# Kernel tuning notes

Hardware: AMD Instinct MI355X
Metric: run time of the kernel (lower is better)

The kernel has to match this reference:

```python
import jax, jax.numpy as jnp
import numpy as np

B, S, D = 64, 64, 2048          # NOTE: repo's RoPE transpose requires B == S
H, KVH, HD = 8, 1, 256
INTER = 16384
EPS = 1e-6
ROPE_THETA = 10000.0


def setup_inputs() -> dict:
    key = jax.random.key(0)
    ks = jax.random.split(key, 10)
    sc = 0.02
    hidden_states = jax.random.normal(ks[0], (B, S, D), jnp.float32)
    causal = jnp.tril(jnp.ones((S, S), dtype=bool))
    attention_mask = jnp.broadcast_to(
        jnp.where(causal, 0.0, -1e9).astype(jnp.float32)[None, None], (B, 1, S, S))
    position_ids = jnp.broadcast_to(jnp.arange(S, dtype=jnp.int32)[None, :], (B, S))
    inv_freq = 1.0 / (ROPE_THETA ** (jnp.arange(0, HD, 2, dtype=jnp.float32) / HD))
    return {
        "hidden_states": hidden_states,
        "attention_mask": attention_mask,
        "position_ids": position_ids,
        "inv_freq": inv_freq,
        "wq": sc * jax.random.normal(ks[1], (H * HD, D), jnp.float32),
        "wk": sc * jax.random.normal(ks[2], (KVH * HD, D), jnp.float32),
        "wv": sc * jax.random.normal(ks[3], (KVH * HD, D), jnp.float32),
        "wo": sc * jax.random.normal(ks[4], (D, H * HD), jnp.float32),
        "w_gate": sc * jax.random.normal(ks[5], (INTER, D), jnp.float32),
        "w_up": sc * jax.random.normal(ks[6], (INTER, D), jnp.float32),
        "w_down": sc * jax.random.normal(ks[7], (D, INTER), jnp.float32),
        "ln1_w": sc * jax.random.normal(ks[8], (D,), jnp.float32),
        "ln2_w": sc * jax.random.normal(ks[9], (D,), jnp.float32),
    }


def _rms_norm(x, w):
    xf = x.astype(jnp.float32)
    out = xf * jax.lax.rsqrt(jnp.mean(xf * xf, axis=-1, keepdims=True) + EPS)
    return (out * (1.0 + w.astype(jnp.float32))).astype(x.dtype)


def _rotate_half(x):
    x1, x2 = jnp.split(x, 2, axis=-1)
    return jnp.concatenate((-x2, x1), axis=-1)


def _decoder_layer(hidden_states, attention_mask, position_ids, inv_freq,
                   wq, wk, wv, wo, w_gate, w_up, w_down, ln1_w, ln2_w):
    residual = hidden_states
    h = _rms_norm(hidden_states, ln1_w)

    # projections -> (B, heads, S, HD)
    q = (h @ wq.T).reshape(B, S, H, HD).transpose(0, 2, 1, 3)
    k = (h @ wk.T).reshape(B, S, KVH, HD).transpose(0, 2, 1, 3)
    v = (h @ wv.T).reshape(B, S, KVH, HD).transpose(0, 2, 1, 3)

    # rotary embeddings: freqs (B, S, HD/2) -> emb (B, S, HD)
    freqs = jnp.einsum('d,bs->bsd', inv_freq, position_ids.astype(jnp.float32))
    emb = jnp.concatenate((freqs, freqs), axis=-1)
    cos, sin = jnp.cos(emb), jnp.sin(emb)
    # faithful to repo: unsqueeze(1) then transpose dims 0<->2 -> (S, 1, B, HD)
    ct = jnp.transpose(cos[:, None], (2, 1, 0, 3))
    st = jnp.transpose(sin[:, None], (2, 1, 0, 3))
    q = q * ct + _rotate_half(q) * st
    k = k * ct + _rotate_half(k) * st

    # repeat_kv: MQA -> full heads
    k = jnp.repeat(k, H // KVH, axis=1)
    v = jnp.repeat(v, H // KVH, axis=1)

    scores = jnp.einsum('bhqd,bhkd->bhqk', q, k) / np.sqrt(HD).astype(np.float32)
    scores = scores + attention_mask
    # softmax computed in float16, then cast back (matches torch code)
    attn = jax.nn.softmax(scores.astype(jnp.float16), axis=-1).astype(q.dtype)

    out = jnp.einsum('bhqk,bhkd->bhqd', attn, v)
    out = out.transpose(0, 2, 1, 3).reshape(B, S, H * HD) @ wo.T
    hidden_states = residual + out

    residual = hidden_states
    h2 = _rms_norm(hidden_states, ln2_w)
    mlp = (jax.nn.gelu(h2 @ w_gate.T, approximate=True) * (h2 @ w_up.T)) @ w_down.T
    hidden_states = residual + mlp
    return hidden_states, attn


def reference(hidden_states, attention_mask, position_ids, inv_freq,
              wq, wk, wv, wo, w_gate, w_up, w_down, ln1_w, ln2_w):
    return _decoder_layer(hidden_states, attention_mask, position_ids, inv_freq,
                          wq, wk, wv, wo, w_gate, w_up, w_down, ln1_w, ln2_w)
```

## Files before the change

kernel.cpp:

```cpp
#include <hip/hip_runtime.h>
#include <hip/hip_fp16.h>

typedef _Float16 half8 __attribute__((ext_vector_type(8)));
typedef _Float16 half4v __attribute__((ext_vector_type(4)));
typedef float floatx4 __attribute__((ext_vector_type(4)));

constexpr int BATCH = 64, SEQ = 64, DM = 2048, NHEAD = 8, HDIM = 256, FF = 16384;

__device__ __forceinline__ float f16r(float x) { return (float)(_Float16)x; }

__global__ __launch_bounds__(256) void rmsnorm_kernel(
    const float* __restrict__ x, const float* __restrict__ w, _Float16* __restrict__ out) {
  const int row = blockIdx.x;
  const float4* xr = (const float4*)(x + (size_t)row * DM);
  const int tid = threadIdx.x;
  float4 a = xr[tid];
  float4 b = xr[tid + 256];
  float s = a.x*a.x + a.y*a.y + a.z*a.z + a.w*a.w
          + b.x*b.x + b.y*b.y + b.z*b.z + b.w*b.w;
  #pragma unroll
  for (int off = 32; off > 0; off >>= 1) s += __shfl_xor(s, off, 64);
  __shared__ float ps[4];
  if ((tid & 63) == 0) ps[tid >> 6] = s;
  __syncthreads();
  const float rs = rsqrtf((ps[0] + ps[1] + ps[2] + ps[3]) * (1.0f / DM) + 1e-6f);
  const float4* wr = (const float4*)w;
  float4 w1 = wr[tid], w2 = wr[tid + 256];
  half4v o1, o2;
  o1[0] = (_Float16)(a.x * rs * (1.f + w1.x));
  o1[1] = (_Float16)(a.y * rs * (1.f + w1.y));
  o1[2] = (_Float16)(a.z * rs * (1.f + w1.z));
  o1[3] = (_Float16)(a.w * rs * (1.f + w1.w));
  o2[0] = (_Float16)(b.x * rs * (1.f + w2.x));
  o2[1] = (_Float16)(b.y * rs * (1.f + w2.y));
  o2[2] = (_Float16)(b.z * rs * (1.f + w2.z));
  o2[3] = (_Float16)(b.w * rs * (1.f + w2.w));
  half4v* op = (half4v*)(out + (size_t)row * DM);
  op[tid] = o1;
  op[tid + 256] = o2;
}

template<int EPI>
__global__ __launch_bounds__(256, 2) void gemm_f16(
    const _Float16* __restrict__ A, const float* __restrict__ Bw,
    float* C, const float* Res, int N, int K) {
  const int m0 = blockIdx.x * 128;
  const int n0 = blockIdx.y * 128;
  __shared__ _Float16 As[128 * 40];
  __shared__ _Float16 Bs[128 * 40];
  const int tid = threadIdx.x;
  const int lane = tid & 63;
  const int wave = tid >> 6;
  const int wm = (wave >> 1) * 64, wn = (wave & 1) * 64;
  const int lr = lane & 15, lk = (lane >> 4) * 8;
  const int r2 = tid >> 1, kh = (tid & 1) * 16;
  const _Float16* Ag = A + (size_t)(m0 + r2) * K + kh;
  const float* Bg = Bw + (size_t)(n0 + r2) * K + kh;
  _Float16* AsW = &As[r2 * 40 + kh];
  _Float16* BsW = &Bs[r2 * 40 + kh];
  floatx4 acc[4][4];
  #pragma unroll
  for (int i = 0; i < 4; ++i)
    #pragma unroll
    for (int j = 0; j < 4; ++j) acc[i][j] = (floatx4){0.f, 0.f, 0.f, 0.f};

  for (int kt = 0; kt < K; kt += 32) {
    float4 a0 = *(const float4*)(Ag);
    float4 a1 = *(const float4*)(Ag + 8);
    float4 b0 = *(const float4*)(Bg);
    float4 b1 = *(const float4*)(Bg + 4);
    float4 b2 = *(const float4*)(Bg + 8);
    float4 b3 = *(const float4*)(Bg + 12);
    Ag += 32; Bg += 32;
    half8 hb0, hb1;
    hb0[0]=(_Float16)b0.x; hb0[1]=(_Float16)b0.y; hb0[2]=(_Float16)b0.z; hb0[3]=(_Float16)b0.w;
    hb0[4]=(_Float16)b1.x; hb0[5]=(_Float16)b1.y; hb0[6]=(_Float16)b1.z; hb0[7]=(_Float16)b1.w;
    hb1[0]=(_Float16)b2.x; hb1[1]=(_Float16)b2.y; hb1[2]=(_Float16)b2.z; hb1[3]=(_Float16)b2.w;
    hb1[4]=(_Float16)b3.x; hb1[5]=(_Float16)b3.y; hb1[6]=(_Float16)b3.z; hb1[7]=(_Float16)b3.w;
    __syncthreads();
    *(float4*)AsW = a0;
    *(float4*)(AsW + 8) = a1;
    *(half8*)BsW = hb0;
    *(half8*)(BsW + 8) = hb1;
    __syncthreads();
    half8 af[4], bfr[4];
    #pragma unroll
    for (int i = 0; i < 4; ++i) af[i] = *(const half8*)&As[(wm + i * 16 + lr) * 40 + lk];
    #pragma unroll
    for (int j = 0; j < 4; ++j) bfr[j] = *(const half8*)&Bs[(wn + j * 16 + lr) * 40 + lk];
    #pragma unroll
    for (int i = 0; i < 4; ++i)
      #pragma unroll
      for (int j = 0; j < 4; ++j)
        acc[i][j] = __builtin_amdgcn_mfma_f32_16x16x32_f16(af[i], bfr[j], acc[i][j], 0, 0, 0);
  }
  const int mb = m0 + wm + (lane >> 4) * 4;
  const int nb = n0 + wn + (lane & 15);
  #pragma unroll
  for (int i = 0; i < 4; ++i)
    #pragma unroll
    for (int j = 0; j < 4; ++j)
      #pragma unroll
      for (int r = 0; r < 4; ++r) {
        size_t idx = (size_t)(mb + i * 16 + r) * N + (nb + j * 16);
        float val = acc[i][j][r];
        if constexpr (EPI == 1) val += Res[idx];
        C[idx] = val;
      }
}

__device__ __forceinline__ float gelu_tanh(float x) {
  float x3 = x * x * x;
  float t = tanhf(0.7978845608028654f * (x + 0.044715f * x3));
  return 0.5f * x * (1.0f + t);
}

__global__ __launch_bounds__(256, 2) void gemm_gateup(
    const _Float16* __restrict__ A, const float* __restrict__ Wg,
    const float* __restrict__ Wu, _Float16* __restrict__ Act) {
  const int K = DM, N = FF;
  const int m0 = blockIdx.x * 128;
  const int n0 = blockIdx.y * 128;
  __shared__ _Float16 As[128 * 40];
  __shared__ _Float16 Bgs[128 * 40];
  __shared__ _Float16 Bus[128 * 40];
  const int tid = threadIdx.x;
  const int lane = tid & 63;
  const int wave = tid >> 6;
  const int wm = (wave >> 1) * 64, wn = (wave & 1) * 64;
  const int lr = lane & 15, lk = (lane >> 4) * 8;
  const int r2 = tid >> 1, kh = (tid & 1) * 16;
  const _Float16* Ag = A + (size_t)(m0 + r2) * K + kh;
  const float* Bgg = Wg + (size_t)(n0 + r2) * K + kh;
  const float* Bgu = Wu + (size_t)(n0 + r2) * K + kh;
  _Float16* AsW = &As[r2 * 40 + kh];
  _Float16* BgW = &Bgs[r2 * 40 + kh];
  _Float16* BuW = &Bus[r2 * 40 + kh];
  floatx4 ag[4][4], au[4][4];
  #pragma unroll
  for (int i = 0; i < 4; ++i)
    #pragma unroll
    for (int j = 0; j < 4; ++j) {
      ag[i][j] = (floatx4){0.f, 0.f, 0.f, 0.f};
      au[i][j] = (floatx4){0.f, 0.f, 0.f, 0.f};
    }
  for (int kt = 0; kt < K; kt += 32) {
    float4 a0 = *(const float4*)(Ag);
    float4 a1 = *(const float4*)(Ag + 8);
    float4 g0 = *(const float4*)(Bgg);
    float4 g1 = *(const float4*)(Bgg + 4);
    float4 g2 = *(const float4*)(Bgg + 8);
    float4 g3 = *(const float4*)(Bgg + 12);
    float4 u0 = *(const float4*)(Bgu);
    float4 u1 = *(const float4*)(Bgu + 4);
    float4 u2 = *(const float4*)(Bgu + 8);
    float4 u3 = *(const float4*)(Bgu + 12);
    Ag += 32; Bgg += 32; Bgu += 32;
    half8 hg0, hg1, hu0, hu1;
    hg0[0]=(_Float16)g0.x; hg0[1]=(_Float16)g0.y; hg0[2]=(_Float16)g0.z; hg0[3]=(_Float16)g0.w;
    hg0[4]=(_Float16)g1.x; hg0[5]=(_Float16)g1.y; hg0[6]=(_Float16)g1.z; hg0[7]=(_Float16)g1.w;
    hg1[0]=(_Float16)g2.x; hg1[1]=(_Float16)g2.y; hg1[2]=(_Float16)g2.z; hg1[3]=(_Float16)g2.w;
    hg1[4]=(_Float16)g3.x; hg1[5]=(_Float16)g3.y; hg1[6]=(_Float16)g3.z; hg1[7]=(_Float16)g3.w;
    hu0[0]=(_Float16)u0.x; hu0[1]=(_Float16)u0.y; hu0[2]=(_Float16)u0.z; hu0[3]=(_Float16)u0.w;
    hu0[4]=(_Float16)u1.x; hu0[5]=(_Float16)u1.y; hu0[6]=(_Float16)u1.z; hu0[7]=(_Float16)u1.w;
    hu1[0]=(_Float16)u2.x; hu1[1]=(_Float16)u2.y; hu1[2]=(_Float16)u2.z; hu1[3]=(_Float16)u2.w;
    hu1[4]=(_Float16)u3.x; hu1[5]=(_Float16)u3.y; hu1[6]=(_Float16)u3.z; hu1[7]=(_Float16)u3.w;
    __syncthreads();
    *(float4*)AsW = a0;
    *(float4*)(AsW + 8) = a1;
    *(half8*)BgW = hg0; *(half8*)(BgW + 8) = hg1;
    *(half8*)BuW = hu0; *(half8*)(BuW + 8) = hu1;
    __syncthreads();
    half8 af[4], bg[4], bu[4];
    #pragma unroll
    for (int i = 0; i < 4; ++i) af[i] = *(const half8*)&As[(wm + i * 16 + lr) * 40 + lk];
    #pragma unroll
    for (int j = 0; j < 4; ++j) {
      bg[j] = *(const half8*)&Bgs[(wn + j * 16 + lr) * 40 + lk];
      bu[j] = *(const half8*)&Bus[(wn + j * 16 + lr) * 40 + lk];
    }
    #pragma unroll
    for (int i = 0; i < 4; ++i)
      #pragma unroll
      for (int j = 0; j < 4; ++j) {
        ag[i][j] = __builtin_amdgcn_mfma_f32_16x16x32_f16(af[i], bg[j], ag[i][j], 0, 0, 0);
        au[i][j] = __builtin_amdgcn_mfma_f32_16x16x32_f16(af[i], bu[j], au[i][j], 0, 0, 0);
      }
  }
  const int mb = m0 + wm + (lane >> 4) * 4;
  const int nb = n0 + wn + (lane & 15);
  #pragma unroll
  for (int i = 0; i < 4; ++i)
    #pragma unroll
    for (int j = 0; j < 4; ++j)
      #pragma unroll
      for (int r = 0; r < 4; ++r) {
        size_t idx = (size_t)(mb + i * 16 + r) * FF + (nb + j * 16);
        Act[idx] = (_Float16)(gelu_tanh(ag[i][j][r]) * au[i][j][r]);
      }
}

__global__ __launch_bounds__(256) void rope_kernel(
    float* __restrict__ x, const int* __restrict__ pos_ids,
    const float* __restrict__ inv_freq, int nh, int total) {
  int tid = blockIdx.x * 256 + threadIdx.x;
  if (tid >= total) return;
  int i = tid & 127;
  int rest = tid >> 7;
  int hh = rest % nh;
  int m = rest / nh;
  int b = m >> 6, s = m & 63;
  int pos = pos_ids[s * 64 + b];
  float fr = inv_freq[i] * (float)pos;
  float c = cosf(fr), sn = sinf(fr);
  size_t base = (size_t)m * ((size_t)nh * 256) + (size_t)hh * 256 + i;
  float x1 = x[base], x2 = x[base + 128];
  x[base] = x1 * c - x2 * sn;
  x[base + 128] = x2 * c + x1 * sn;
}

__global__ __launch_bounds__(256) void attn_kernel(
    const float* __restrict__ q, const float* __restrict__ k, const float* __restrict__ v,
    const float* __restrict__ mask, float* __restrict__ attn_out, _Float16* __restrict__ ctx) {
  const int bh = blockIdx.x;
  const int b = bh >> 3, h = bh & 7;
  __shared__ __align__(16) char smem[65536];
  const int tid = threadIdx.x;
  for (int it = 0; it < 16; ++it) {
    int f = it * 256 + tid;
    int t = f >> 6, d4 = f & 63;
    float4 kv = *(const float4*)(k + (size_t)(b * 64 + t) * HDIM + d4 * 4);
    int col = d4 ^ ((t >> 2) & 7);
    *(float4*)(smem + t * 1024 + col * 16) = kv;
  }
  __syncthreads();
  const int sg = tid >> 4, tg = tid & 15;
  const int s0 = sg * 4, t0 = tg * 4;
  float sc[4][4] = {};
  const float* qb = q + (size_t)(b * 64 + s0) * DM + h * HDIM;
  for (int d4 = 0; d4 < 64; ++d4) {
    float4 kvv[4];
    int col = d4 ^ (tg & 7);
    #pragma unroll
    for (int j = 0; j < 4; ++j)
      kvv[j] = *(const float4*)(smem + (t0 + j) * 1024 + col * 16);
    #pragma unroll
    for (int i = 0; i < 4; ++i) {
      float4 qv = *(const float4*)(qb + (size_t)i * DM + d4 * 4);
      #pragma unroll
      for (int j = 0; j < 4; ++j)
        sc[i][j] += qv.x * kvv[j].x + qv.y * kvv[j].y + qv.z * kvv[j].z + qv.w * kvv[j].w;
    }
  }
  float a16[4][4];
  const float* mrow = mask + (size_t)b * SEQ * SEQ;
  #pragma unroll
  for (int i = 0; i < 4; ++i) {
    const float4 mk = *(const float4*)(mrow + (size_t)(s0 + i) * SEQ + t0);
    float xh[4];
    xh[0] = f16r(sc[i][0] * 0.0625f + mk.x);
    xh[1] = f16r(sc[i][1] * 0.0625f + mk.y);
    xh[2] = f16r(sc[i][2] * 0.0625f + mk.z);
    xh[3] = f16r(sc[i][3] * 0.0625f + mk.w);
    float mx = fmaxf(fmaxf(xh[0], xh[1]), fmaxf(xh[2], xh[3]));
    #pragma unroll
    for (int off = 1; off < 16; off <<= 1) mx = fmaxf(mx, __shfl_xor(mx, off, 64));
    float ssum = 0.f;
    #pragma unroll
    for (int j = 0; j < 4; ++j) {
      float e = f16r(expf(f16r(xh[j] - mx)));
      a16[i][j] = e;
      ssum += e;
    }
    #pragma unroll
    for (int off = 1; off < 16; off <<= 1) ssum += __shfl_xor(ssum, off, 64);
    #pragma unroll
    for (int j = 0; j < 4; ++j) a16[i][j] = f16r(a16[i][j] / ssum);
  }
  float* ab = attn_out + (size_t)bh * SEQ * SEQ;
  #pragma unroll
  for (int i = 0; i < 4; ++i) {
    float4 av = {a16[i][0], a16[i][1], a16[i][2], a16[i][3]};
    *(float4*)(ab + (size_t)(s0 + i) * SEQ + t0) = av;
  }
  __syncthreads();
  float* as = (float*)smem;
  _Float16* vs = (_Float16*)(smem + 64 * 65 * 4);
  #pragma unroll
  for (int i = 0; i < 4; ++i)
    #pragma unroll
    for (int j = 0; j < 4; ++j)
      as[(s0 + i) * 65 + t0 + j] = a16[i][j];
  for (int it = 0; it < 16; ++it) {
    int f = it * 256 + tid;
    int t = f >> 6, d4 = f & 63;
    float4 vv = *(const float4*)(v + (size_t)(b * 64 + t) * HDIM + d4 * 4);
    half4v hv;
    hv[0] = (_Float16)vv.x; hv[1] = (_Float16)vv.y;
    hv[2] = (_Float16)vv.z; hv[3] = (_Float16)vv.w;
    *(half4v*)(vs + t * 264 + d4 * 4) = hv;
  }
  __syncthreads();
  floatx4 outv[4][4];
  #pragma unroll
  for (int i = 0; i < 4; ++i)
    #pragma unroll
    for (int u = 0; u < 4; ++u) outv[i][u] = (floatx4){0.f, 0.f, 0.f, 0.f};
  for (int t = 0; t < 64; ++t) {
    float av[4];
    #pragma unroll
    for (int i = 0; i < 4; ++i) av[i] = as[(s0 + i) * 65 + t];
    #pragma unroll
    for (int u = 0; u < 4; ++u) {
      half4v vh = *(const half4v*)(vs + t * 264 + tg * 4 + u * 64);
      floatx4 vf = {(float)vh[0], (float)vh[1], (float)vh[2], (float)vh[3]};
      #pragma unroll
      for (int i = 0; i < 4; ++i) outv[i][u] += vf * av[i];
    }
  }
  #pragma unroll
  for (int i = 0; i < 4; ++i)
    #pragma unroll
    for (int u = 0; u < 4; ++u) {
      half4v hv;
      hv[0] = (_Float16)outv[i][u][0];
      hv[1] = (_Float16)outv[i][u][1];
      hv[2] = (_Float16)outv[i][u][2];
      hv[3] = (_Float16)outv[i][u][3];
      *(half4v*)(ctx + (size_t)(b * 64 + s0 + i) * DM + h * HDIM + u * 64 + tg * 4) = hv;
    }
}

extern "C" void kernel_launch(void* const* d_in, const int* in_sizes, int n_in,
                              void* d_out, int out_size, void* d_ws, size_t ws_size,
                              hipStream_t stream) {
  const float* hs   = (const float*)d_in[0];
  const float* mask = (const float*)d_in[1];
  const int*   pos  = (const int*)d_in[2];
  const float* invf = (const float*)d_in[3];
  const float* wq   = (const float*)d_in[4];
  const float* wk   = (const float*)d_in[5];
  const float* wv   = (const float*)d_in[6];
  const float* wo   = (const float*)d_in[7];
  const float* wg   = (const float*)d_in[8];
  const float* wu   = (const float*)d_in[9];
  const float* wd   = (const float*)d_in[10];
  const float* ln1  = (const float*)d_in[11];
  const float* ln2  = (const float*)d_in[12];

  float* out_hidden = (float*)d_out;
  float* out_attn   = out_hidden + 8388608;

  char* ws = (char*)d_ws;
  _Float16* h_half = (_Float16*)ws;
  char* Creg = ws + (size_t)16777216;
  float*     qb  = (float*)(Creg);
  float*     kb  = (float*)(Creg + 33554432);
  float*     vb  = (float*)(Creg + 37748736);
  _Float16*  ctx = (_Float16*)(Creg + 41943040);
  _Float16*  act = (_Float16*)(Creg);

  rmsnorm_kernel<<<4096, 256, 0, stream>>>(hs, ln1, h_half);
  gemm_f16<0><<<dim3(32, 16), 256, 0, stream>>>(h_half, wq, qb, nullptr, 2048, 2048);
  gemm_f16<0><<<dim3(32, 2),  256, 0, stream>>>(h_half, wk, kb, nullptr, 256, 2048);
  gemm_f16<0><<<dim3(32, 2),  256, 0, stream>>>(h_half, wv, vb, nullptr, 256, 2048);
  rope_kernel<<<16384, 256, 0, stream>>>(qb, pos, invf, 8, 4096 * 8 * 128);
  rope_kernel<<<2048,  256, 0, stream>>>(kb, pos, invf, 1, 4096 * 1 * 128);
  attn_kernel<<<512, 256, 0, stream>>>(qb, kb, vb, mask, out_attn, ctx);
  gemm_f16<1><<<dim3(32, 16), 256, 0, stream>>>(ctx, wo, out_hidden, hs, 2048, 2048);
  rmsnorm_kernel<<<4096, 256, 0, stream>>>(out_hidden, ln2, h_half);
  gemm_gateup<<<dim3(32, 128), 256, 0, stream>>>(h_half, wg, wu, act);
  gemm_f16<1><<<dim3(32, 16), 256, 0, stream>>>(act, wd, out_hidden, out_hidden, 2048, 16384);
}
```

Measured before the change: 2.252 ms.

## Pre-convert weights to fp16 and stream tiles via global_load_lds GEMMs

Adds a path, used when the workspace is large enough, that first converts every fp32 weight matrix to fp16 in a separate kernel. New GEMM kernels then load A and B tiles straight into LDS with global_load_lds instead of converting per block inside the K loop. Q, K and V are fused into one GEMM with a shared 2560-wide output, so RoPE and attention now take a leading-dimension argument. GELU is rewritten with exp instead of tanhf. The conversions add a full extra pass over the weights each call, the new GEMMs are single-buffered with two barriers per K step, and the old path remains as a fallback.

```diff
diff --git a/kernel.cpp b/kernel.cpp
--- a/kernel.cpp
+++ b/kernel.cpp
@@ -8,6 +8,30 @@
 constexpr int BATCH = 64, SEQ = 64, DM = 2048, NHEAD = 8, HDIM = 256, FF = 16384;
 
 __device__ __forceinline__ float f16r(float x) { return (float)(_Float16)x; }
+
+__device__ __forceinline__ void gld_lds16(const _Float16* g, _Float16* l) {
+  __builtin_amdgcn_global_load_lds(
+      (const __attribute__((address_space(1))) void*)g,
+      (__attribute__((address_space(3))) void*)l, 16, 0, 0);
+}
+
+__device__ __forceinline__ float gelu_tanh(float x) {
+  float z = 1.5957691216057308f * (x + 0.044715f * x * x * x);
+  float t = __expf(z);
+  return 0.5f * x * (1.0f + (t - 1.0f) / (t + 1.0f));
+}
+
+__global__ __launch_bounds__(256) void convert_f16(
+    const float* __restrict__ s, _Float16* __restrict__ d, int n8) {
+  int t = blockIdx.x * 256 + threadIdx.x;
+  if (t >= n8) return;
+  const float4* sp = (const float4*)s + (size_t)t * 2;
+  float4 x = sp[0], y = sp[1];
+  half8 h;
+  h[0] = (_Float16)x.x; h[1] = (_Float16)x.y; h[2] = (_Float16)x.z; h[3] = (_Float16)x.w;
+  h[4] = (_Float16)y.x; h[5] = (_Float16)y.y; h[6] = (_Float16)y.z; h[7] = (_Float16)y.w;
+  ((half8*)d)[t] = h;
+}
 
 __global__ __launch_bounds__(256) void rmsnorm_kernel(
     const float* __restrict__ x, const float* __restrict__ w, _Float16* __restrict__ out) {
@@ -41,6 +65,135 @@
 }
 
 template<int EPI>
+__global__ __launch_bounds__(256) void gemm_lds(
+    const _Float16* __restrict__ A, const _Float16* __restrict__ B,
+    float* C, const float* __restrict__ Res, int N, int K) {
+  __shared__ _Float16 As[128 * 32];
+  __shared__ _Float16 Bs[128 * 32];
+  const int tid = threadIdx.x;
+  const int lane = tid & 63, wave = tid >> 6;
+  const int m0 = blockIdx.x * 128, n0 = blockIdx.y * 128;
+  const int wm = (wave >> 1) * 64, wn = (wave & 1) * 64;
+  const int lr = lane & 15, lk = (lane >> 4) * 8;
+  const int srow = wave * 32 + (lane >> 2);
+  const int scol = (lane & 3) * 8;
+  const _Float16* Ag0 = A + (size_t)(m0 + srow) * K + scol;
+  const _Float16* Ag1 = Ag0 + (size_t)16 * K;
+  const _Float16* Bg0 = B + (size_t)(n0 + srow) * K + scol;
+  const _Float16* Bg1 = Bg0 + (size_t)16 * K;
+  _Float16* lA0 = As + wave * 1024;
+  _Float16* lA1 = As + wave * 1024 + 512;
+  _Float16* lB0 = Bs + wave * 1024;
+  _Float16* lB1 = Bs + wave * 1024 + 512;
+  floatx4 acc[4][4];
+  #pragma unroll
+  for (int i = 0; i < 4; ++i)
+    #pragma unroll
+    for (int j = 0; j < 4; ++j) acc[i][j] = (floatx4){0.f, 0.f, 0.f, 0.f};
+
+  for (int kt = 0; kt < K; kt += 32) {
+    gld_lds16(Ag0 + kt, lA0);
+    gld_lds16(Ag1 + kt, lA1);
+    gld_lds16(Bg0 + kt, lB0);
+    gld_lds16(Bg1 + kt, lB1);
+    __syncthreads();
+    half8 af[4], bf[4];
+    #pragma unroll
+    for (int i = 0; i < 4; ++i) af[i] = *(const half8*)&As[(wm + i * 16 + lr) * 32 + lk];
+    #pragma unroll
+    for (int j = 0; j < 4; ++j) bf[j] = *(const half8*)&Bs[(wn + j * 16 + lr) * 32 + lk];
+    #pragma unroll
+    for (int i = 0; i < 4; ++i)
+      #pragma unroll
+      for (int j = 0; j < 4; ++j)
+        acc[i][j] = __builtin_amdgcn_mfma_f32_16x16x32_f16(af[i], bf[j], acc[i][j], 0, 0, 0);
+    __syncthreads();
+  }
+  const int mb = m0 + wm + (lane >> 4) * 4;
+  const int nb = n0 + wn + (lane & 15);
+  #pragma unroll
+  for (int i = 0; i < 4; ++i)
+    #pragma unroll
+    for (int j = 0; j < 4; ++j)
+      #pragma unroll
+      for (int r = 0; r < 4; ++r) {
+        size_t idx = (size_t)(mb + i * 16 + r) * N + (nb + j * 16);
+        float val = acc[i][j][r];
+        if constexpr (EPI == 1) val += Res[idx];
+        C[idx] = val;
+      }
+}
+
+__global__ __launch_bounds__(256) void gateup_lds(
+    const _Float16* __restrict__ A, const _Float16* __restrict__ Wg,
+    const _Float16* __restrict__ Wu, _Float16* __restrict__ Act) {
+  const int K = DM;
+  __shared__ _Float16 As[128 * 32];
+  __shared__ _Float16 Gs[128 * 32];
+  __shared__ _Float16 Us[128 * 32];
+  const int tid = threadIdx.x;
+  const int lane = tid & 63, wave = tid >> 6;
+  const int m0 = blockIdx.x * 128, n0 = blockIdx.y * 128;
+  const int wm = (wave >> 1) * 64, wn = (wave & 1) * 64;
+  const int lr = lane & 15, lk = (lane >> 4) * 8;
+  const int srow = wave * 32 + (lane >> 2);
+  const int scol = (lane & 3) * 8;
+  const _Float16* Ag0 = A + (size_t)(m0 + srow) * K + scol;
+  const _Float16* Ag1 = Ag0 + (size_t)16 * K;
+  const _Float16* Gg0 = Wg + (size_t)(n0 + srow) * K + scol;
+  const _Float16* Gg1 = Gg0 + (size_t)16 * K;
+  const _Float16* Ug0 = Wu + (size_t)(n0 + srow) * K + scol;
+  const _Float16* Ug1 = Ug0 + (size_t)16 * K;
+  _Float16* lA0 = As + wave * 1024; _Float16* lA1 = lA0 + 512;
+  _Float16* lG0 = Gs + wave * 1024; _Float16* lG1 = lG0 + 512;
+  _Float16* lU0 = Us + wave * 1024; _Float16* lU1 = lU0 + 512;
+  floatx4 ag[4][4], au[4][4];
+  #pragma unroll
+  for (int i = 0; i < 4; ++i)
+    #pragma unroll
+    for (int j = 0; j < 4; ++j) {
+      ag[i][j] = (floatx4){0.f, 0.f, 0.f, 0.f};
+      au[i][j] = (floatx4){0.f, 0.f, 0.f, 0.f};
+    }
+  for (int kt = 0; kt < K; kt += 32) {
+    gld_lds16(Ag0 + kt, lA0);
+    gld_lds16(Ag1 + kt, lA1);
+    gld_lds16(Gg0 + kt, lG0);
+    gld_lds16(Gg1 + kt, lG1);
+    gld_lds16(Ug0 + kt, lU0);
+    gld_lds16(Ug1 + kt, lU1);
+    __syncthreads();
+    half8 af[4], bg[4], bu[4];
+    #pragma unroll
+    for (int i = 0; i < 4; ++i) af[i] = *(const half8*)&As[(wm + i * 16 + lr) * 32 + lk];
+    #pragma unroll
+    for (int j = 0; j < 4; ++j) {
+      bg[j] = *(const half8*)&Gs[(wn + j * 16 + lr) * 32 + lk];
+      bu[j] = *(const half8*)&Us[(wn + j * 16 + lr) * 32 + lk];
+    }
+    #pragma unroll
+    for (int i = 0; i < 4; ++i)
+      #pragma unroll
+      for (int j = 0; j < 4; ++j) {
+        ag[i][j] = __builtin_amdgcn_mfma_f32_16x16x32_f16(af[i], bg[j], ag[i][j], 0, 0, 0);
+        au[i][j] = __builtin_amdgcn_mfma_f32_16x16x32_f16(af[i], bu[j], au[i][j], 0, 0, 0);
+      }
+    __syncthreads();
+  }
+  const int mb = m0 + wm + (lane >> 4) * 4;
+  const int nb = n0 + wn + (lane & 15);
+  #pragma unroll
+  for (int i = 0; i < 4; ++i)
+    #pragma unroll
+    for (int j = 0; j < 4; ++j)
+      #pragma unroll
+      for (int r = 0; r < 4; ++r) {
+        size_t idx = (size_t)(mb + i * 16 + r) * FF + (nb + j * 16);
+        Act[idx] = (_Float16)(gelu_tanh(ag[i][j][r]) * au[i][j][r]);
+      }
+}
+
+template<int EPI>
 __global__ __launch_bounds__(256, 2) void gemm_f16(
     const _Float16* __restrict__ A, const float* __restrict__ Bw,
     float* C, const float* Res, int N, int K) {
@@ -63,7 +216,6 @@
   for (int i = 0; i < 4; ++i)
     #pragma unroll
     for (int j = 0; j < 4; ++j) acc[i][j] = (floatx4){0.f, 0.f, 0.f, 0.f};
-
   for (int kt = 0; kt < K; kt += 32) {
     float4 a0 = *(const float4*)(Ag);
     float4 a1 = *(const float4*)(Ag + 8);
@@ -109,16 +261,10 @@
       }
 }
 
-__device__ __forceinline__ float gelu_tanh(float x) {
-  float x3 = x * x * x;
-  float t = tanhf(0.7978845608028654f * (x + 0.044715f * x3));
-  return 0.5f * x * (1.0f + t);
-}
-
 __global__ __launch_bounds__(256, 2) void gemm_gateup(
     const _Float16* __restrict__ A, const float* __restrict__ Wg,
     const float* __restrict__ Wu, _Float16* __restrict__ Act) {
-  const int K = DM, N = FF;
+  const int K = DM;
   const int m0 = blockIdx.x * 128;
   const int n0 = blockIdx.y * 128;
   __shared__ _Float16 As[128 * 40];
@@ -202,7 +348,7 @@
 
 __global__ __launch_bounds__(256) void rope_kernel(
     float* __restrict__ x, const int* __restrict__ pos_ids,
-    const float* __restrict__ inv_freq, int nh, int total) {
+    const float* __restrict__ inv_freq, int nh, int ld, int total) {
   int tid = blockIdx.x * 256 + threadIdx.x;
   if (tid >= total) return;
   int i = tid & 127;
@@ -213,14 +359,16 @@
   int pos = pos_ids[s * 64 + b];
   float fr = inv_freq[i] * (float)pos;
   float c = cosf(fr), sn = sinf(fr);
-  size_t base = (size_t)m * ((size_t)nh * 256) + (size_t)hh * 256 + i;
+  size_t base = (size_t)m * ld + (size_t)hh * 256 + i;
   float x1 = x[base], x2 = x[base + 128];
   x[base] = x1 * c - x2 * sn;
   x[base + 128] = x2 * c + x1 * sn;
 }
 
 __global__ __launch_bounds__(256) void attn_kernel(
-    const float* __restrict__ q, const float* __restrict__ k, const float* __restrict__ v,
+    const float* __restrict__ qbase, int qld,
+    const float* __restrict__ kbase, int kld,
+    const float* __restrict__ vbase, int vld,
     const float* __restrict__ mask, float* __restrict__ attn_out, _Float16* __restrict__ ctx) {
   const int bh = blockIdx.x;
   const int b = bh >> 3, h = bh & 7;
@@ -229,7 +377,7 @@
   for (int it = 0; it < 16; ++it) {
     int f = it * 256 + tid;
     int t = f >> 6, d4 = f & 63;
-    float4 kv = *(const float4*)(k + (size_t)(b * 64 + t) * HDIM + d4 * 4);
+    float4 kv = *(const float4*)(kbase + (size_t)(b * 64 + t) * kld + d4 * 4);
     int col = d4 ^ ((t >> 2) & 7);
     *(float4*)(smem + t * 1024 + col * 16) = kv;
   }
@@ -237,7 +385,7 @@
   const int sg = tid >> 4, tg = tid & 15;
   const int s0 = sg * 4, t0 = tg * 4;
   float sc[4][4] = {};
-  const float* qb = q + (size_t)(b * 64 + s0) * DM + h * HDIM;
+  const float* qb = qbase + (size_t)(b * 64 + s0) * qld + h * HDIM;
   for (int d4 = 0; d4 < 64; ++d4) {
     float4 kvv[4];
     int col = d4 ^ (tg & 7);
@@ -246,7 +394,7 @@
       kvv[j] = *(const float4*)(smem + (t0 + j) * 1024 + col * 16);
     #pragma unroll
     for (int i = 0; i < 4; ++i) {
-      float4 qv = *(const float4*)(qb + (size_t)i * DM + d4 * 4);
+      float4 qv = *(const float4*)(qb + (size_t)i * qld + d4 * 4);
       #pragma unroll
       for (int j = 0; j < 4; ++j)
         sc[i][j] += qv.x * kvv[j].x + qv.y * kvv[j].y + qv.z * kvv[j].z + qv.w * kvv[j].w;
@@ -294,7 +442,7 @@
   for (int it = 0; it < 16; ++it) {
     int f = it * 256 + tid;
     int t = f >> 6, d4 = f & 63;
-    float4 vv = *(const float4*)(v + (size_t)(b * 64 + t) * HDIM + d4 * 4);
+    float4 vv = *(const float4*)(vbase + (size_t)(b * 64 + t) * vld + d4 * 4);
     half4v hv;
     hv[0] = (_Float16)vv.x; hv[1] = (_Float16)vv.y;
     hv[2] = (_Float16)vv.z; hv[3] = (_Float16)vv.w;
@@ -351,24 +499,57 @@
   float* out_hidden = (float*)d_out;
   float* out_attn   = out_hidden + 8388608;
 
+  const size_t FULL_NEED = 352321536;
   char* ws = (char*)d_ws;
-  _Float16* h_half = (_Float16*)ws;
-  char* Creg = ws + (size_t)16777216;
-  float*     qb  = (float*)(Creg);
-  float*     kb  = (float*)(Creg + 33554432);
-  float*     vb  = (float*)(Creg + 37748736);
-  _Float16*  ctx = (_Float16*)(Creg + 41943040);
-  _Float16*  act = (_Float16*)(Creg);
-
-  rmsnorm_kernel<<<4096, 256, 0, stream>>>(hs, ln1, h_half);
-  gemm_f16<0><<<dim3(32, 16), 256, 0, stream>>>(h_half, wq, qb, nullptr, 2048, 2048);
-  gemm_f16<0><<<dim3(32, 2),  256, 0, stream>>>(h_half, wk, kb, nullptr, 256, 2048);
-  gemm_f16<0><<<dim3(32, 2),  256, 0, stream>>>(h_half, wv, vb, nullptr, 256, 2048);
-  rope_kernel<<<16384, 256, 0, stream>>>(qb, pos, invf, 8, 4096 * 8 * 128);
-  rope_kernel<<<2048,  256, 0, stream>>>(kb, pos, invf, 1, 4096 * 1 * 128);
-  attn_kernel<<<512, 256, 0, stream>>>(qb, kb, vb, mask, out_attn, ctx);
-  gemm_f16<1><<<dim3(32, 16), 256, 0, stream>>>(ctx, wo, out_hidden, hs, 2048, 2048);
-  rmsnorm_kernel<<<4096, 256, 0, stream>>>(out_hidden, ln2, h_half);
-  gemm_gateup<<<dim3(32, 128), 256, 0, stream>>>(h_half, wg, wu, act);
-  gemm_f16<1><<<dim3(32, 16), 256, 0, stream>>>(act, wd, out_hidden, out_hidden, 2048, 16384);
-}
+
+  if (ws_size >= FULL_NEED) {
+    _Float16* h_half = (_Float16*)(ws);
+    _Float16* wg_h   = (_Float16*)(ws + 16777216);
+    _Float16* wu_h   = (_Float16*)(ws + 83886080);
+    _Float16* wd_h   = (_Float16*)(ws + 150994944);
+    char*     rx     = ws + 218103808;
+    _Float16* qkvw   = (_Float16*)(rx);
+    _Float16* wo_h   = (_Float16*)(rx + 10485760);
+    float*    qkv    = (float*)(rx + 18874368);
+    _Float16* ctx    = (_Float16*)(rx + 60817408);
+    _Float16* act    = (_Float16*)(rx);
+
+    convert_f16<<<2048, 256, 0, stream>>>(wq, qkvw, 524288);
+    convert_f16<<<256,  256, 0, stream>>>(wk, qkvw + (size_t)2048 * 2048, 65536);
+    convert_f16<<<256,  256, 0, stream>>>(wv, qkvw + (size_t)2304 * 2048, 65536);
+    convert_f16<<<2048, 256, 0, stream>>>(wo, wo_h, 524288);
+    convert_f16<<<16384, 256, 0, stream>>>(wg, wg_h, 4194304);
+    convert_f16<<<16384, 256, 0, stream>>>(wu, wu_h, 4194304);
+    convert_f16<<<16384, 256, 0, stream>>>(wd, wd_h, 4194304);
+
+    rmsnorm_kernel<<<4096, 256, 0, stream>>>(hs, ln1, h_half);
+    gemm_lds<0><<<dim3(32, 20), 256, 0, stream>>>(h_half, qkvw, qkv, nullptr, 2560, 2048);
+    rope_kernel<<<18432, 256, 0, stream>>>(qkv, pos, invf, 9, 2560, 4096 * 9 * 128);
+    attn_kernel<<<512, 256, 0, stream>>>(qkv, 2560, qkv + 2048, 2560, qkv + 2304, 2560,
+                                         mask, out_attn, ctx);
+    gemm_lds<1><<<dim3(32, 16), 256, 0, stream>>>(ctx, wo_h, out_hidden, hs, 2048, 2048);
+    rmsnorm_kernel<<<4096, 256, 0, stream>>>(out_hidden, ln2, h_half);
+    gateup_lds<<<dim3(32, 128), 256, 0, stream>>>(h_half, wg_h, wu_h, act);
+    gemm_lds<1><<<dim3(32, 16), 256, 0, stream>>>(act, wd_h, out_hidden, out_hidden, 2048, 16384);
+  } else {
+    _Float16* h_half = (_Float16*)ws;
+    char* Creg = ws + (size_t)16777216;
+    float*     qb  = (float*)(Creg);
+    float*     kb  = (float*)(Creg + 33554432);
+    float*     vb  = (float*)(Creg + 37748736);
+    _Float16*  ctx = (_Float16*)(Creg + 41943040);
+    _Float16*  act = (_Float16*)(Creg);
+
+    rmsnorm_kernel<<<4096, 256, 0, stream>>>(hs, ln1, h_half);
+    gemm_f16<0><<<dim3(32, 16), 256, 0, stream>>>(h_half, wq, qb, nullptr, 2048, 2048);
+    gemm_f16<0><<<dim3(32, 2),  256, 0, stream>>>(h_half, wk, kb, nullptr, 256, 2048);
+    gemm_f16<0><<<dim3(32, 2),  256, 0, stream>>>(h_half, wv, vb, nullptr, 256, 2048);
+    rope_kernel<<<16384, 256, 0, stream>>>(qb, pos, invf, 8, 2048, 4096 * 8 * 128);
+    rope_kernel<<<2048,  256, 0, stream>>>(kb, pos, invf, 1, 256, 4096 * 1 * 128);
+    attn_kernel<<<512, 256, 0, stream>>>(qb, 2048, kb, 256, vb, 256, mask, out_attn, ctx);
+    gemm_f16<1><<<dim3(32, 16), 256, 0, stream>>>(ctx, wo, out_hidden, hs, 2048, 2048);
+    rmsnorm_kernel<<<4096, 256, 0, stream>>>(out_hidden, ln2, h_half);
+    gemm_gateup<<<dim3(32, 128), 256, 0, stream>>>(h_half, wg, wu, act);
+    gemm_f16<1><<<dim3(32, 16), 256, 0, stream>>>(act, wd, out_hidden, out_hidden, 2048, 16384);
+  }
+}
```

Measured after the change: 2.284 ms. No clear change (+1.4%).
